# Performance work log

Hardware: AMD Instinct MI355X
Metric: run time of the kernel (lower is better)

## Reference

```python
import jax, jax.numpy as jnp
import numpy as np

B, I, H, O, K = 256, 512, 512, 512, 256


def setup_inputs() -> dict:
    key = jax.random.key(0)
    ks = jax.random.split(key, 16)
    def lin(kw, kb, out_dim, in_dim):
        s = 1.0 / np.sqrt(in_dim)
        W = jax.random.uniform(kw, (out_dim, in_dim), jnp.float32, -s, s)
        b = jax.random.uniform(kb, (out_dim,), jnp.float32, -s, s)
        return W, b
    Wd, bd = lin(ks[0], ks[1], H, I + 2 * H)
    Wr, br = lin(ks[2], ks[3], H, I + H)
    Wz, bz = lin(ks[4], ks[5], H, I + H)
    Wh, bh = lin(ks[6], ks[7], H, I + H)
    Wo, bo = lin(ks[8], ks[9], O, H)
    return {
        "sample": jax.random.normal(ks[10], (B, I), jnp.float32),
        "hidden": jax.random.normal(ks[11], (B, H), jnp.float32),
        "hidden_tensor": jax.random.normal(ks[12], (K, B, H), jnp.float32),
        "d_0": jax.random.normal(ks[13], (B, H), jnp.float32),
        "Wd": Wd, "bd": bd, "Wr": Wr, "br": br,
        "Wz": Wz, "bz": bz, "Wh": Wh, "bh": bh, "Wo": Wo, "bo": bo,
    }


def _filter_d(hidden_tensor, d_values):
    # get_ws: w[j] = prod_{m=0}^{K-1-j} (m - d) / (m + 1)  for j in [0, K)
    # Vectorized: cumprod of (m-d)/(m+1) along m, then flip.
    m = jnp.arange(K, dtype=d_values.dtype).reshape(K, 1, 1)  # [K,1,1]
    factors = (m - d_values[None, :, :]) / (m + 1.0)          # [K,B,H]
    w = jnp.flip(jnp.cumprod(factors, axis=0), axis=0)        # [K,B,H]
    return jnp.sum(hidden_tensor * w, axis=0)                 # [B,H]


def reference(sample, hidden, hidden_tensor, d_0,
              Wd, bd, Wr, br, Wz, bz, Wh, bh, Wo, bo):
    combined = jnp.concatenate([sample, hidden], axis=1)          # [B, I+H]
    combined_d = jnp.concatenate([sample, hidden, d_0], axis=1)   # [B, I+2H]

    d_values = jax.nn.sigmoid(combined_d @ Wd.T + bd) * 0.5       # [B,H]
    first = -_filter_d(hidden_tensor, d_values)                   # [B,H]

    r_gate = jax.nn.sigmoid(combined @ Wr.T + br)
    z_gate = jax.nn.sigmoid(combined @ Wz.T + bz)

    combined2 = jnp.concatenate([sample, r_gate * hidden], axis=1)
    h_tilde = jnp.tanh(combined2 @ Wh.T + bh)
    second = h_tilde * (1.0 - z_gate)

    hidden_new = first + second                                   # [B,H]
    h_c_1 = jnp.concatenate([hidden_tensor, hidden_new[None]], axis=0)[1:]  # [K,B,H]
    output = hidden_new @ Wo.T + bo                               # [B,O]
    return (output, hidden_new, h_c_1, d_values)
```

## Files before the change

### kernel.cpp

```cpp
#include <hip/hip_runtime.h>

#define B_ 256
#define H_ 512
#define KF 256
#define BH 131072
#define BH4 32768
#define H4 128

#define BM 64
#define BN 64
#define BK 16

__device__ __forceinline__ float sigmoidf_(float x) { return 1.0f / (1.0f + __expf(-x)); }
__device__ __forceinline__ float tanh_fast(float x) { return 2.0f / (1.0f + __expf(-2.0f * x)) - 1.0f; }
__device__ __forceinline__ float4 sig4(float4 v) {
    return make_float4(sigmoidf_(v.x), sigmoidf_(v.y), sigmoidf_(v.z), sigmoidf_(v.w));
}

template<bool MUL>
__device__ __forceinline__ void gemm64(
    float (*As)[BM + 4], float (*Ws)[BN + 4],
    const float* __restrict__ abase, const float* __restrict__ rbase,
    const float* __restrict__ W, int Ktot, int ks,
    int bm, int bn, int nIter, float* __restrict__ p)
{
    const int tid = threadIdx.x;
    const int ty = tid >> 4, tx = tid & 15;
    const int lrow = tid >> 2, lcol = (tid & 3) << 2;
    const float* aptr = abase + (bm + lrow) * 512 + lcol;
    const float* rptr = MUL ? rbase + (bm + lrow) * 512 + lcol : nullptr;
    const float* wptr = W + (size_t)(bn + lrow) * Ktot + ks + lcol;

    float acc[4][4] = {};
    float4 av = *(const float4*)aptr;
    if (MUL) { const float4 rv = *(const float4*)rptr;
               av.x *= rv.x; av.y *= rv.y; av.z *= rv.z; av.w *= rv.w; }
    float4 wv = *(const float4*)wptr;

    for (int it = 0; it < nIter; ++it) {
        __syncthreads();
        As[lcol + 0][lrow] = av.x; As[lcol + 1][lrow] = av.y;
        As[lcol + 2][lrow] = av.z; As[lcol + 3][lrow] = av.w;
        Ws[lcol + 0][lrow] = wv.x; Ws[lcol + 1][lrow] = wv.y;
        Ws[lcol + 2][lrow] = wv.z; Ws[lcol + 3][lrow] = wv.w;
        __syncthreads();
        if (it < nIter - 1) {
            av = *(const float4*)(aptr + (it + 1) * BK);
            if (MUL) { const float4 rv = *(const float4*)(rptr + (it + 1) * BK);
                       av.x *= rv.x; av.y *= rv.y; av.z *= rv.z; av.w *= rv.w; }
            wv = *(const float4*)(wptr + (it + 1) * BK);
        }
        #pragma unroll
        for (int kk = 0; kk < BK; ++kk) {
            const float4 a = *(const float4*)&As[kk][ty << 2];
            const float4 w = *(const float4*)&Ws[kk][tx << 2];
            const float a4[4] = {a.x, a.y, a.z, a.w};
            const float w4[4] = {w.x, w.y, w.z, w.w};
            #pragma unroll
            for (int i = 0; i < 4; ++i)
                #pragma unroll
                for (int j = 0; j < 4; ++j)
                    acc[i][j] = fmaf(a4[i], w4[j], acc[i][j]);
        }
    }
    #pragma unroll
    for (int i = 0; i < 4; ++i) {
        const int m = bm + (ty << 2) + i;
        #pragma unroll
        for (int j = 0; j < 4; ++j)
            p[m * 512 + bn + (tx << 2) + j] = acc[i][j];
    }
}

__global__ __launch_bounds__(256) void k_gemm_d(
    const float* __restrict__ sample, const float* __restrict__ hidden,
    const float* __restrict__ d0, const float* __restrict__ Wd,
    float* __restrict__ parts)
{
    __shared__ float As[BK][BM + 4];
    __shared__ float Ws[BK][BN + 4];
    const int s = blockIdx.z, ks = s << 8, seg = ks >> 9;
    const float* ab = (seg == 0 ? sample : (seg == 1 ? hidden : d0)) + (ks & 511);
    gemm64<false>(As, Ws, ab, nullptr, Wd, 1536, ks,
                  blockIdx.y * BM, blockIdx.x * BN, 16, parts + (size_t)s * BH);
}

__global__ __launch_bounds__(256) void k_mega1(
    const float* __restrict__ ht, const float* dparts, const float* __restrict__ bd,
    const float* __restrict__ sample, const float* __restrict__ hidden,
    const float* __restrict__ Wr, const float* __restrict__ Wz,
    float* __restrict__ rzparts, float* __restrict__ dv_out,
    float* hc1, float* __restrict__ cst, float* __restrict__ accst)
{
    if (blockIdx.x >= 512) {
        __shared__ float As[BK][BM + 4];
        __shared__ float Ws[BK][BN + 4];
        const int id = blockIdx.x - 512;
        const int gz = id >> 7, rem = id & 127;
        const int s = rem >> 5, t2 = rem & 31;
        const int bn = (t2 >> 2) << 6, bm = (t2 & 3) << 6, ks = s << 8;
        const float* ab = (ks < 512 ? sample + ks : hidden + (ks - 512));
        gemm64<false>(As, Ws, ab, nullptr, gz ? Wz : Wr, 1024, ks, bm, bn, 16,
                      rzparts + (size_t)(gz * 4 + s) * BH);
        return;
    }
    __shared__ float s_inv[128], s_tinv[128];
    const int tid = threadIdx.x;
    if (tid < 128) { const float fi = 1.0f / (float)(tid + 1);
                     s_inv[tid] = fi; s_tinv[tid] = (float)tid * fi; }
    __syncthreads();

    const int g = blockIdx.x * 256 + tid;
    const int n = g & (H_ - 1);
    float sd = bd[n];
    #pragma unroll
    for (int s = 0; s < 6; ++s) sd += dparts[(size_t)s * BH + g];
    const float d = 0.5f * sigmoidf_(sd);
    dv_out[g] = d;

    float c = 1.0f, acc = 0.0f;
    #pragma unroll 8
    for (int t = 0; t < 128; ++t) {
        const int k = 255 - t;
        const float v = ht[(size_t)k * BH + g];
        c *= fmaf(-d, s_inv[t], s_tinv[t]);
        acc = fmaf(v, c, acc);
        hc1[(size_t)(k - 1) * BH + g] = v;
    }
    cst[g] = c; accst[g] = acc;
}

__global__ __launch_bounds__(256) void k_reduce_rz(
    const float4* __restrict__ parts, const float4* __restrict__ br,
    const float4* __restrict__ bz, float4* __restrict__ rb, float4* __restrict__ zb)
{
    const int g = blockIdx.x * 256 + threadIdx.x;
    const int n = g & (H4 - 1);
    float4 r = br[n], z = bz[n];
    #pragma unroll
    for (int s = 0; s < 4; ++s) { const float4 p = parts[(size_t)s * BH4 + g];
        r.x += p.x; r.y += p.y; r.z += p.z; r.w += p.w; }
    #pragma unroll
    for (int s = 4; s < 8; ++s) { const float4 p = parts[(size_t)s * BH4 + g];
        z.x += p.x; z.y += p.y; z.z += p.z; z.w += p.w; }
    rb[g] = sig4(r); zb[g] = sig4(z);
}

__global__ __launch_bounds__(256) void k_mega2(
    const float* __restrict__ ht, const float* __restrict__ dv,
    const float* __restrict__ sample, const float* __restrict__ hidden,
    const float* __restrict__ rb, const float* __restrict__ Wh,
    float* __restrict__ hparts, float* hc1,
    const float* __restrict__ cst, float* __restrict__ accst)
{
    if (blockIdx.x >= 512) {
        __shared__ float As[BK][BM + 4];
        __shared__ float Ws[BK][BN + 4];
        const int id = blockIdx.x - 512;
        const int s = id >> 5, t2 = id & 31;
        const int bn = (t2 >> 2) << 6, bm = (t2 & 3) << 6, ks = s << 8;
        if (ks < 512)
            gemm64<false>(As, Ws, sample + ks, nullptr, Wh, 1024, ks, bm, bn, 16,
                          hparts + (size_t)s * BH);
        else
            gemm64<true>(As, Ws, hidden + (ks - 512), rb + (ks - 512), Wh, 1024, ks,
                         bm, bn, 16, hparts + (size_t)s * BH);
        return;
    }
    __shared__ float s_inv[128], s_tinv[128];
    const int tid = threadIdx.x;
    if (tid < 128) { const int t = tid + 128; const float fi = 1.0f / (float)(t + 1);
                     s_inv[tid] = fi; s_tinv[tid] = (float)t * fi; }
    __syncthreads();

    const int g = blockIdx.x * 256 + tid;
    const float d = dv[g];
    float c = cst[g], acc = accst[g];
    #pragma unroll 8
    for (int t = 0; t < 128; ++t) {
        const int k = 127 - t;
        const float v = ht[(size_t)k * BH + g];
        c *= fmaf(-d, s_inv[t], s_tinv[t]);
        acc = fmaf(v, c, acc);
        if (k >= 1) hc1[(size_t)(k - 1) * BH + g] = v;
    }
    accst[g] = acc;
}

__global__ __launch_bounds__(256) void k_finalize(
    const float4* __restrict__ hparts, const float4* __restrict__ bh,
    const float4* __restrict__ zb, const float4* __restrict__ accst,
    float4* __restrict__ hn_out, float4* __restrict__ hc1_4)
{
    const int g = blockIdx.x * 256 + threadIdx.x;
    const int n = g & (H4 - 1);
    float4 sh = bh[n];
    #pragma unroll
    for (int s = 0; s < 4; ++s) { const float4 p = hparts[(size_t)s * BH4 + g];
        sh.x += p.x; sh.y += p.y; sh.z += p.z; sh.w += p.w; }
    const float4 z = zb[g], a = accst[g];
    float4 hn;
    hn.x = tanh_fast(sh.x) * (1.0f - z.x) - a.x;
    hn.y = tanh_fast(sh.y) * (1.0f - z.y) - a.y;
    hn.z = tanh_fast(sh.z) * (1.0f - z.z) - a.z;
    hn.w = tanh_fast(sh.w) * (1.0f - z.w) - a.w;
    hn_out[g] = hn;
    hc1_4[(size_t)255 * BH4 + g] = hn;
}

__global__ __launch_bounds__(256) void k_gemm_o(
    const float* __restrict__ hn, const float* __restrict__ Wo,
    float* __restrict__ parts, int chunk)
{
    __shared__ float As[BK][BM + 4];
    __shared__ float Ws[BK][BN + 4];
    const int s = blockIdx.z, ks = s * chunk;
    gemm64<false>(As, Ws, hn + ks, nullptr, Wo, 512, ks,
                  blockIdx.y * BM, blockIdx.x * BN, chunk / BK, parts + (size_t)s * BH);
}

__global__ __launch_bounds__(256) void k_reduce_o(
    const float4* parts, const float4* __restrict__ bo, float4* out, int NS)
{
    const int g = blockIdx.x * 256 + threadIdx.x;
    float4 v = bo[g & (H4 - 1)];
    for (int s = 0; s < NS; ++s) { const float4 p = parts[(size_t)s * BH4 + g];
        v.x += p.x; v.y += p.y; v.z += p.z; v.w += p.w; }
    out[g] = v;
}

__global__ __launch_bounds__(256) void k_gemm_rz(
    const float* __restrict__ sample, const float* __restrict__ hidden,
    const float* __restrict__ Wr, const float* __restrict__ Wz,
    float* __restrict__ parts)
{
    __shared__ float As[BK][BM + 4];
    __shared__ float Ws[BK][BN + 4];
    const int z = blockIdx.z, gz = z >> 2, s = z & 3, ks = s << 8;
    const float* ab = (ks < 512 ? sample + ks : hidden + (ks - 512));
    gemm64<false>(As, Ws, ab, nullptr, gz ? Wz : Wr, 1024, ks,
                  blockIdx.y * BM, blockIdx.x * BN, 16, parts + (size_t)z * BH);
}

__global__ __launch_bounds__(256) void k_gemm_h(
    const float* __restrict__ sample, const float* __restrict__ hidden,
    const float* __restrict__ rb, const float* __restrict__ Wh,
    float* __restrict__ parts)
{
    __shared__ float As[BK][BM + 4];
    __shared__ float Ws[BK][BN + 4];
    const int s = blockIdx.z, ks = s << 8;
    if (ks < 512)
        gemm64<false>(As, Ws, sample + ks, nullptr, Wh, 1024, ks,
                      blockIdx.y * BM, blockIdx.x * BN, 16, parts + (size_t)s * BH);
    else
        gemm64<true>(As, Ws, hidden + (ks - 512), rb + (ks - 512), Wh, 1024, ks,
                     blockIdx.y * BM, blockIdx.x * BN, 16, parts + (size_t)s * BH);
}

__global__ __launch_bounds__(256) void k_filter_full(
    const float* __restrict__ ht, const float* dparts, const float* __restrict__ bd,
    const float* zbuf, const float* hparts, const float* __restrict__ bh,
    float* hc1, float* __restrict__ dv_out, float* __restrict__ hn_out)
{
    __shared__ float s_inv[KF], s_tinv[KF];
    const int tid = threadIdx.x;
    const float fi = 1.0f / (float)(tid + 1);
    s_inv[tid] = fi; s_tinv[tid] = (float)tid * fi;
    __syncthreads();

    const int g = blockIdx.x * 256 + tid;
    const int n = g & (H_ - 1);
    float sd = bd[n];
    #pragma unroll
    for (int s = 0; s < 6; ++s) sd += dparts[(size_t)s * BH + g];
    const float d = 0.5f * sigmoidf_(sd);
    dv_out[g] = d;
    float sh = bh[n];
    #pragma unroll
    for (int s = 0; s < 4; ++s) sh += hparts[(size_t)s * BH + g];
    const float z = zbuf[g];

    float c = 1.0f, acc = 0.0f;
    #pragma unroll 8
    for (int t = 0; t < KF; ++t) {
        const int k = KF - 1 - t;
        const float v = ht[(size_t)k * BH + g];
        c *= fmaf(-d, s_inv[t], s_tinv[t]);
        acc = fmaf(v, c, acc);
        if (k >= 1) hc1[(size_t)(k - 1) * BH + g] = v;
    }
    const float hn = tanh_fast(sh) * (1.0f - z) - acc;
    hc1[(size_t)(KF - 1) * BH + g] = hn;
    hn_out[g] = hn;
}

extern "C" void kernel_launch(void* const* d_in, const int* in_sizes, int n_in,
                              void* d_out, int out_size, void* d_ws, size_t ws_size,
                              hipStream_t stream)
{
    const float* sample = (const float*)d_in[0];
    const float* hidden = (const float*)d_in[1];
    const float* ht     = (const float*)d_in[2];
    const float* d0     = (const float*)d_in[3];
    const float* Wd = (const float*)d_in[4];
    const float* bd = (const float*)d_in[5];
    const float* br = (const float*)d_in[7];
    const float* Wr = (const float*)d_in[6];
    const float* Wz = (const float*)d_in[8];
    const float* bz = (const float*)d_in[9];
    const float* Wh = (const float*)d_in[10];
    const float* bh = (const float*)d_in[11];
    const float* Wo = (const float*)d_in[12];
    const float* bo = (const float*)d_in[13];

    float* out     = (float*)d_out;
    float* out_o   = out;
    float* out_hn  = out + BH;
    float* out_hc1 = out + 2 * BH;
    float* out_dv  = out + 2 * BH + (size_t)KF * BH;

    const size_t slice = BH;
    const size_t need = 12ull * slice * sizeof(float);

    if (ws_size >= need) {
        float* ws  = (float*)d_ws;
        float* rz  = ws;
        float* hp  = ws;
        float* op  = ws + 4 * slice;
        float* rb  = ws + 8 * slice;
        float* zb  = ws + 9 * slice;
        float* cst = ws + 10 * slice;
        float* acc = ws + 11 * slice;
        float* dpar = out_hc1;

        k_gemm_d<<<dim3(8, 4, 6), 256, 0, stream>>>(sample, hidden, d0, Wd, dpar);
        k_mega1<<<dim3(768), 256, 0, stream>>>(ht, dpar, bd, sample, hidden, Wr, Wz,
                                               rz, out_dv, out_hc1, cst, acc);
        k_reduce_rz<<<dim3(128), 256, 0, stream>>>((const float4*)rz, (const float4*)br,
                                                   (const float4*)bz, (float4*)rb, (float4*)zb);
        k_mega2<<<dim3(640), 256, 0, stream>>>(ht, out_dv, sample, hidden, rb, Wh,
                                               hp, out_hc1, cst, acc);
        k_finalize<<<dim3(128), 256, 0, stream>>>((const float4*)hp, (const float4*)bh,
                                                  (const float4*)zb, (const float4*)acc,
                                                  (float4*)out_hn, (float4*)out_hc1);
        k_gemm_o<<<dim3(8, 4, 4), 256, 0, stream>>>(out_hn, Wo, op, 128);
        k_reduce_o<<<dim3(128), 256, 0, stream>>>((const float4*)op, (const float4*)bo,
                                                  (float4*)out_o, 4);
    } else {
        float* sl = out_hc1;
        k_gemm_d<<<dim3(8, 4, 6), 256, 0, stream>>>(sample, hidden, d0, Wd, sl);
        k_gemm_rz<<<dim3(8, 4, 8), 256, 0, stream>>>(sample, hidden, Wr, Wz, sl + 6 * slice);
        k_reduce_rz<<<dim3(128), 256, 0, stream>>>((const float4*)(sl + 6 * slice),
                                                   (const float4*)br, (const float4*)bz,
                                                   (float4*)(sl + 14 * slice),
                                                   (float4*)(sl + 15 * slice));
        k_gemm_h<<<dim3(8, 4, 4), 256, 0, stream>>>(sample, hidden, sl + 14 * slice, Wh,
                                                    sl + 16 * slice);
        k_filter_full<<<dim3(512), 256, 0, stream>>>(ht, sl, bd, sl + 15 * slice,
                                                     sl + 16 * slice, bh,
                                                     out_hc1, out_dv, out_hn);
        k_gemm_o<<<dim3(8, 4, 1), 256, 0, stream>>>(out_hn, Wo, out_o, 512);
        k_reduce_o<<<dim3(128), 256, 0, stream>>>((const float4*)out_o, (const float4*)bo,
                                                  (float4*)out_o, 1);
    }
}
```

Baseline: 89.92 us.

## Merge d/r/z GEMMs into one launch and fuse the filter into a single pass

Moves the d, r and z split-K GEMMs into a single launch and merges the two half-filter mega kernels into one kernel. That kernel runs the Wh GEMM blocks alongside the full 256-step filter. The r-gate reduction and sigmoid are folded into the Wh GEMM's A-tile load, and the z reduction moves into finalize, which removes k_reduce_rz and the cst/acc intermediates. The aim is fewer launches and less global round-tripping. In exchange, the filter's full 256-step chain now sits in only 512 blocks, and each r load re-reduces four partials per GEMM tile.

After: 92.79 us. +3.2%, slower.

```diff
diff --git a/kernel.cpp b/kernel.cpp
--- a/kernel.cpp
+++ b/kernel.cpp
@@ -16,6 +16,20 @@
 __device__ __forceinline__ float4 sig4(float4 v) {
     return make_float4(sigmoidf_(v.x), sigmoidf_(v.y), sigmoidf_(v.z), sigmoidf_(v.w));
 }
+
+#define MAC_LOOP()                                                         \
+    _Pragma("unroll")                                                      \
+    for (int kk = 0; kk < BK; ++kk) {                                      \
+        const float4 a = *(const float4*)&As[kk][ty << 2];                 \
+        const float4 w = *(const float4*)&Ws[kk][tx << 2];                 \
+        const float a4[4] = {a.x, a.y, a.z, a.w};                          \
+        const float w4[4] = {w.x, w.y, w.z, w.w};                          \
+        _Pragma("unroll")                                                  \
+        for (int i = 0; i < 4; ++i)                                        \
+            _Pragma("unroll")                                              \
+            for (int j = 0; j < 4; ++j)                                    \
+                acc[i][j] = fmaf(a4[i], w4[j], acc[i][j]);                 \
+    }
 
 template<bool MUL>
 __device__ __forceinline__ void gemm64(
@@ -50,18 +64,7 @@
                        av.x *= rv.x; av.y *= rv.y; av.z *= rv.z; av.w *= rv.w; }
             wv = *(const float4*)(wptr + (it + 1) * BK);
         }
-        #pragma unroll
-        for (int kk = 0; kk < BK; ++kk) {
-            const float4 a = *(const float4*)&As[kk][ty << 2];
-            const float4 w = *(const float4*)&Ws[kk][tx << 2];
-            const float a4[4] = {a.x, a.y, a.z, a.w};
-            const float w4[4] = {w.x, w.y, w.z, w.w};
-            #pragma unroll
-            for (int i = 0; i < 4; ++i)
-                #pragma unroll
-                for (int j = 0; j < 4; ++j)
-                    acc[i][j] = fmaf(a4[i], w4[j], acc[i][j]);
-        }
+        MAC_LOOP();
     }
     #pragma unroll
     for (int i = 0; i < 4; ++i) {
@@ -72,138 +75,152 @@
     }
 }
 
-__global__ __launch_bounds__(256) void k_gemm_d(
+__device__ __forceinline__ void gemm64_rmul(
+    float (*As)[BM + 4], float (*Ws)[BN + 4],
+    const float* __restrict__ hidden, const float* __restrict__ rparts,
+    const float* __restrict__ br, const float* __restrict__ W,
+    int ks, int bm, int bn, float* __restrict__ p)
+{
+    const int tid = threadIdx.x;
+    const int ty = tid >> 4, tx = tid & 15;
+    const int lrow = tid >> 2, lcol = (tid & 3) << 2;
+    const int off = ks - 512;
+    const float* aptr = hidden + (bm + lrow) * 512 + off + lcol;
+    const float* rptr = rparts + (bm + lrow) * 512 + off + lcol;
+    const float* bptr = br + off + lcol;
+    const float* wptr = W + (size_t)(bn + lrow) * 1024 + ks + lcol;
+
+    float acc[4][4] = {};
+    float4 av, wv;
+    {
+        float4 rs = *(const float4*)bptr;
+        #pragma unroll
+        for (int s = 0; s < 4; ++s) { const float4 rp = *(const float4*)(rptr + (size_t)s * BH);
+            rs.x += rp.x; rs.y += rp.y; rs.z += rp.z; rs.w += rp.w; }
+        const float4 hv = *(const float4*)aptr;
+        av = make_float4(sigmoidf_(rs.x) * hv.x, sigmoidf_(rs.y) * hv.y,
+                         sigmoidf_(rs.z) * hv.z, sigmoidf_(rs.w) * hv.w);
+        wv = *(const float4*)wptr;
+    }
+    for (int it = 0; it < 16; ++it) {
+        __syncthreads();
+        As[lcol + 0][lrow] = av.x; As[lcol + 1][lrow] = av.y;
+        As[lcol + 2][lrow] = av.z; As[lcol + 3][lrow] = av.w;
+        Ws[lcol + 0][lrow] = wv.x; Ws[lcol + 1][lrow] = wv.y;
+        Ws[lcol + 2][lrow] = wv.z; Ws[lcol + 3][lrow] = wv.w;
+        __syncthreads();
+        if (it < 15) {
+            float4 rs = *(const float4*)(bptr + (it + 1) * BK);
+            #pragma unroll
+            for (int s = 0; s < 4; ++s) { const float4 rp = *(const float4*)(rptr + (size_t)s * BH + (it + 1) * BK);
+                rs.x += rp.x; rs.y += rp.y; rs.z += rp.z; rs.w += rp.w; }
+            const float4 hv = *(const float4*)(aptr + (it + 1) * BK);
+            av = make_float4(sigmoidf_(rs.x) * hv.x, sigmoidf_(rs.y) * hv.y,
+                             sigmoidf_(rs.z) * hv.z, sigmoidf_(rs.w) * hv.w);
+            wv = *(const float4*)(wptr + (it + 1) * BK);
+        }
+        MAC_LOOP();
+    }
+    #pragma unroll
+    for (int i = 0; i < 4; ++i) {
+        const int m = bm + (ty << 2) + i;
+        #pragma unroll
+        for (int j = 0; j < 4; ++j)
+            p[m * 512 + bn + (tx << 2) + j] = acc[i][j];
+    }
+}
+
+__global__ __launch_bounds__(256) void k_gemm_drz(
     const float* __restrict__ sample, const float* __restrict__ hidden,
-    const float* __restrict__ d0, const float* __restrict__ Wd,
-    float* __restrict__ parts)
+    const float* __restrict__ d0,
+    const float* __restrict__ Wd, const float* __restrict__ Wr,
+    const float* __restrict__ Wz,
+    float* __restrict__ dbase, float* __restrict__ rzbase)
 {
     __shared__ float As[BK][BM + 4];
     __shared__ float Ws[BK][BN + 4];
-    const int s = blockIdx.z, ks = s << 8, seg = ks >> 9;
-    const float* ab = (seg == 0 ? sample : (seg == 1 ? hidden : d0)) + (ks & 511);
-    gemm64<false>(As, Ws, ab, nullptr, Wd, 1536, ks,
-                  blockIdx.y * BM, blockIdx.x * BN, 16, parts + (size_t)s * BH);
-}
-
-__global__ __launch_bounds__(256) void k_mega1(
-    const float* __restrict__ ht, const float* dparts, const float* __restrict__ bd,
+    const int z = blockIdx.z;
+    if (z < 6) {
+        const int ks = z << 8, seg = ks >> 9;
+        const float* ab = (seg == 0 ? sample : (seg == 1 ? hidden : d0)) + (ks & 511);
+        gemm64<false>(As, Ws, ab, nullptr, Wd, 1536, ks,
+                      blockIdx.y * BM, blockIdx.x * BN, 16, dbase + (size_t)z * BH);
+    } else {
+        const int id = z - 6, gz = id >> 2, s = id & 3, ks = s << 8;
+        const float* ab = (ks < 512 ? sample + ks : hidden + (ks - 512));
+        gemm64<false>(As, Ws, ab, nullptr, gz ? Wz : Wr, 1024, ks,
+                      blockIdx.y * BM, blockIdx.x * BN, 16, rzbase + (size_t)id * BH);
+    }
+}
+
+__global__ __launch_bounds__(256) void k_mega(
+    const float* __restrict__ ht, const float* __restrict__ bd,
     const float* __restrict__ sample, const float* __restrict__ hidden,
-    const float* __restrict__ Wr, const float* __restrict__ Wz,
-    float* __restrict__ rzparts, float* __restrict__ dv_out,
-    float* hc1, float* __restrict__ cst, float* __restrict__ accst)
-{
-    if (blockIdx.x >= 512) {
+    const float* __restrict__ rparts, const float* __restrict__ br,
+    const float* __restrict__ Wh, float* __restrict__ hparts,
+    float* hc1, float* __restrict__ dv_out)
+{
+    if (blockIdx.x < 128) {
         __shared__ float As[BK][BM + 4];
         __shared__ float Ws[BK][BN + 4];
-        const int id = blockIdx.x - 512;
-        const int gz = id >> 7, rem = id & 127;
-        const int s = rem >> 5, t2 = rem & 31;
-        const int bn = (t2 >> 2) << 6, bm = (t2 & 3) << 6, ks = s << 8;
-        const float* ab = (ks < 512 ? sample + ks : hidden + (ks - 512));
-        gemm64<false>(As, Ws, ab, nullptr, gz ? Wz : Wr, 1024, ks, bm, bn, 16,
-                      rzparts + (size_t)(gz * 4 + s) * BH);
-        return;
-    }
-    __shared__ float s_inv[128], s_tinv[128];
-    const int tid = threadIdx.x;
-    if (tid < 128) { const float fi = 1.0f / (float)(tid + 1);
-                     s_inv[tid] = fi; s_tinv[tid] = (float)tid * fi; }
-    __syncthreads();
-
-    const int g = blockIdx.x * 256 + tid;
-    const int n = g & (H_ - 1);
-    float sd = bd[n];
-    #pragma unroll
-    for (int s = 0; s < 6; ++s) sd += dparts[(size_t)s * BH + g];
-    const float d = 0.5f * sigmoidf_(sd);
-    dv_out[g] = d;
-
-    float c = 1.0f, acc = 0.0f;
-    #pragma unroll 8
-    for (int t = 0; t < 128; ++t) {
-        const int k = 255 - t;
-        const float v = ht[(size_t)k * BH + g];
-        c *= fmaf(-d, s_inv[t], s_tinv[t]);
-        acc = fmaf(v, c, acc);
-        hc1[(size_t)(k - 1) * BH + g] = v;
-    }
-    cst[g] = c; accst[g] = acc;
-}
-
-__global__ __launch_bounds__(256) void k_reduce_rz(
-    const float4* __restrict__ parts, const float4* __restrict__ br,
-    const float4* __restrict__ bz, float4* __restrict__ rb, float4* __restrict__ zb)
-{
-    const int g = blockIdx.x * 256 + threadIdx.x;
-    const int n = g & (H4 - 1);
-    float4 r = br[n], z = bz[n];
-    #pragma unroll
-    for (int s = 0; s < 4; ++s) { const float4 p = parts[(size_t)s * BH4 + g];
-        r.x += p.x; r.y += p.y; r.z += p.z; r.w += p.w; }
-    #pragma unroll
-    for (int s = 4; s < 8; ++s) { const float4 p = parts[(size_t)s * BH4 + g];
-        z.x += p.x; z.y += p.y; z.z += p.z; z.w += p.w; }
-    rb[g] = sig4(r); zb[g] = sig4(z);
-}
-
-__global__ __launch_bounds__(256) void k_mega2(
-    const float* __restrict__ ht, const float* __restrict__ dv,
-    const float* __restrict__ sample, const float* __restrict__ hidden,
-    const float* __restrict__ rb, const float* __restrict__ Wh,
-    float* __restrict__ hparts, float* hc1,
-    const float* __restrict__ cst, float* __restrict__ accst)
-{
-    if (blockIdx.x >= 512) {
-        __shared__ float As[BK][BM + 4];
-        __shared__ float Ws[BK][BN + 4];
-        const int id = blockIdx.x - 512;
+        const int id = blockIdx.x;
         const int s = id >> 5, t2 = id & 31;
         const int bn = (t2 >> 2) << 6, bm = (t2 & 3) << 6, ks = s << 8;
         if (ks < 512)
             gemm64<false>(As, Ws, sample + ks, nullptr, Wh, 1024, ks, bm, bn, 16,
                           hparts + (size_t)s * BH);
         else
-            gemm64<true>(As, Ws, hidden + (ks - 512), rb + (ks - 512), Wh, 1024, ks,
-                         bm, bn, 16, hparts + (size_t)s * BH);
+            gemm64_rmul(As, Ws, hidden, rparts, br, Wh, ks, bm, bn,
+                        hparts + (size_t)s * BH);
         return;
     }
-    __shared__ float s_inv[128], s_tinv[128];
+    __shared__ float s_inv[KF], s_tinv[KF];
     const int tid = threadIdx.x;
-    if (tid < 128) { const int t = tid + 128; const float fi = 1.0f / (float)(t + 1);
-                     s_inv[tid] = fi; s_tinv[tid] = (float)t * fi; }
+    const float fi = 1.0f / (float)(tid + 1);
+    s_inv[tid] = fi; s_tinv[tid] = (float)tid * fi;
     __syncthreads();
 
-    const int g = blockIdx.x * 256 + tid;
-    const float d = dv[g];
-    float c = cst[g], acc = accst[g];
-    #pragma unroll 8
-    for (int t = 0; t < 128; ++t) {
-        const int k = 127 - t;
+    const int g = (blockIdx.x - 128) * 256 + tid;
+    const int n = g & (H_ - 1);
+    float sd = bd[n];
+    #pragma unroll
+    for (int s = 0; s < 6; ++s) sd += hc1[(size_t)s * BH + g];
+    const float d = 0.5f * sigmoidf_(sd);
+    dv_out[g] = d;
+
+    float c = 1.0f, acc = 0.0f;
+    #pragma unroll 16
+    for (int t = 0; t < KF; ++t) {
+        const int k = KF - 1 - t;
         const float v = ht[(size_t)k * BH + g];
         c *= fmaf(-d, s_inv[t], s_tinv[t]);
         acc = fmaf(v, c, acc);
         if (k >= 1) hc1[(size_t)(k - 1) * BH + g] = v;
     }
-    accst[g] = acc;
+    hc1[(size_t)(KF - 1) * BH + g] = acc;
 }
 
 __global__ __launch_bounds__(256) void k_finalize(
+    const float4* __restrict__ zparts, const float4* __restrict__ bz,
     const float4* __restrict__ hparts, const float4* __restrict__ bh,
-    const float4* __restrict__ zb, const float4* __restrict__ accst,
-    float4* __restrict__ hn_out, float4* __restrict__ hc1_4)
+    float4* hc1_4, float4* __restrict__ hn_out)
 {
     const int g = blockIdx.x * 256 + threadIdx.x;
     const int n = g & (H4 - 1);
-    float4 sh = bh[n];
+    float4 zs = bz[n], hs = bh[n];
+    #pragma unroll
+    for (int s = 0; s < 4; ++s) { const float4 p = zparts[(size_t)s * BH4 + g];
+        zs.x += p.x; zs.y += p.y; zs.z += p.z; zs.w += p.w; }
     #pragma unroll
     for (int s = 0; s < 4; ++s) { const float4 p = hparts[(size_t)s * BH4 + g];
-        sh.x += p.x; sh.y += p.y; sh.z += p.z; sh.w += p.w; }
-    const float4 z = zb[g], a = accst[g];
+        hs.x += p.x; hs.y += p.y; hs.z += p.z; hs.w += p.w; }
+    const float4 z = sig4(zs);
+    const float4 a = hc1_4[(size_t)255 * BH4 + g];
     float4 hn;
-    hn.x = tanh_fast(sh.x) * (1.0f - z.x) - a.x;
-    hn.y = tanh_fast(sh.y) * (1.0f - z.y) - a.y;
-    hn.z = tanh_fast(sh.z) * (1.0f - z.z) - a.z;
-    hn.w = tanh_fast(sh.w) * (1.0f - z.w) - a.w;
+    hn.x = tanh_fast(hs.x) * (1.0f - z.x) - a.x;
+    hn.y = tanh_fast(hs.y) * (1.0f - z.y) - a.y;
+    hn.z = tanh_fast(hs.z) * (1.0f - z.z) - a.z;
+    hn.w = tanh_fast(hs.w) * (1.0f - z.w) - a.w;
     hn_out[g] = hn;
     hc1_4[(size_t)255 * BH4 + g] = hn;
 }
@@ -229,17 +246,20 @@
     out[g] = v;
 }
 
-__global__ __launch_bounds__(256) void k_gemm_rz(
-    const float* __restrict__ sample, const float* __restrict__ hidden,
-    const float* __restrict__ Wr, const float* __restrict__ Wz,
-    float* __restrict__ parts)
-{
-    __shared__ float As[BK][BM + 4];
-    __shared__ float Ws[BK][BN + 4];
-    const int z = blockIdx.z, gz = z >> 2, s = z & 3, ks = s << 8;
-    const float* ab = (ks < 512 ? sample + ks : hidden + (ks - 512));
-    gemm64<false>(As, Ws, ab, nullptr, gz ? Wz : Wr, 1024, ks,
-                  blockIdx.y * BM, blockIdx.x * BN, 16, parts + (size_t)z * BH);
+__global__ __launch_bounds__(256) void k_reduce_rz(
+    const float4* __restrict__ parts, const float4* __restrict__ br,
+    const float4* __restrict__ bz, float4* __restrict__ rb, float4* __restrict__ zb)
+{
+    const int g = blockIdx.x * 256 + threadIdx.x;
+    const int n = g & (H4 - 1);
+    float4 r = br[n], z = bz[n];
+    #pragma unroll
+    for (int s = 0; s < 4; ++s) { const float4 p = parts[(size_t)s * BH4 + g];
+        r.x += p.x; r.y += p.y; r.z += p.z; r.w += p.w; }
+    #pragma unroll
+    for (int s = 4; s < 8; ++s) { const float4 p = parts[(size_t)s * BH4 + g];
+        z.x += p.x; z.y += p.y; z.z += p.z; z.w += p.w; }
+    rb[g] = sig4(r); zb[g] = sig4(z);
 }
 
 __global__ __launch_bounds__(256) void k_gemm_h(
@@ -282,7 +302,7 @@
     const float z = zbuf[g];
 
     float c = 1.0f, acc = 0.0f;
-    #pragma unroll 8
+    #pragma unroll 16
     for (int t = 0; t < KF; ++t) {
         const int k = KF - 1 - t;
         const float v = ht[(size_t)k * BH + g];
@@ -305,8 +325,8 @@
     const float* d0     = (const float*)d_in[3];
     const float* Wd = (const float*)d_in[4];
     const float* bd = (const float*)d_in[5];
+    const float* Wr = (const float*)d_in[6];
     const float* br = (const float*)d_in[7];
-    const float* Wr = (const float*)d_in[6];
     const float* Wz = (const float*)d_in[8];
     const float* bz = (const float*)d_in[9];
     const float* Wh = (const float*)d_in[10];
@@ -324,33 +344,25 @@
     const size_t need = 12ull * slice * sizeof(float);
 
     if (ws_size >= need) {
-        float* ws  = (float*)d_ws;
-        float* rz  = ws;
-        float* hp  = ws;
-        float* op  = ws + 4 * slice;
-        float* rb  = ws + 8 * slice;
-        float* zb  = ws + 9 * slice;
-        float* cst = ws + 10 * slice;
-        float* acc = ws + 11 * slice;
-        float* dpar = out_hc1;
-
-        k_gemm_d<<<dim3(8, 4, 6), 256, 0, stream>>>(sample, hidden, d0, Wd, dpar);
-        k_mega1<<<dim3(768), 256, 0, stream>>>(ht, dpar, bd, sample, hidden, Wr, Wz,
-                                               rz, out_dv, out_hc1, cst, acc);
-        k_reduce_rz<<<dim3(128), 256, 0, stream>>>((const float4*)rz, (const float4*)br,
-                                                   (const float4*)bz, (float4*)rb, (float4*)zb);
-        k_mega2<<<dim3(640), 256, 0, stream>>>(ht, out_dv, sample, hidden, rb, Wh,
-                                               hp, out_hc1, cst, acc);
-        k_finalize<<<dim3(128), 256, 0, stream>>>((const float4*)hp, (const float4*)bh,
-                                                  (const float4*)zb, (const float4*)acc,
-                                                  (float4*)out_hn, (float4*)out_hc1);
-        k_gemm_o<<<dim3(8, 4, 4), 256, 0, stream>>>(out_hn, Wo, op, 128);
-        k_reduce_o<<<dim3(128), 256, 0, stream>>>((const float4*)op, (const float4*)bo,
+        float* ws = (float*)d_ws;
+        k_gemm_drz<<<dim3(8, 4, 14), 256, 0, stream>>>(sample, hidden, d0,
+                                                       Wd, Wr, Wz, out_hc1, ws);
+        k_mega<<<dim3(640), 256, 0, stream>>>(ht, bd, sample, hidden,
+                                              ws , br, Wh,
+                                              ws + 8 * slice ,
+                                              out_hc1, out_dv);
+        k_finalize<<<dim3(128), 256, 0, stream>>>(
+            (const float4*)(ws + 4 * slice), (const float4*)bz,
+            (const float4*)(ws + 8 * slice), (const float4*)bh,
+            (float4*)out_hc1, (float4*)out_hn);
+        k_gemm_o<<<dim3(8, 4, 4), 256, 0, stream>>>(out_hn, Wo, ws, 128);
+        k_reduce_o<<<dim3(128), 256, 0, stream>>>((const float4*)ws,
+                                                  (const float4*)bo,
                                                   (float4*)out_o, 4);
     } else {
         float* sl = out_hc1;
-        k_gemm_d<<<dim3(8, 4, 6), 256, 0, stream>>>(sample, hidden, d0, Wd, sl);
-        k_gemm_rz<<<dim3(8, 4, 8), 256, 0, stream>>>(sample, hidden, Wr, Wz, sl + 6 * slice);
+        k_gemm_drz<<<dim3(8, 4, 14), 256, 0, stream>>>(sample, hidden, d0,
+                                                       Wd, Wr, Wz, sl, sl + 6 * slice);
         k_reduce_rz<<<dim3(128), 256, 0, stream>>>((const float4*)(sl + 6 * slice),
                                                    (const float4*)br, (const float4*)bz,
                                                    (float4*)(sl + 14 * slice),
```
